# Kernel optimization log

Hardware: AMD Instinct MI355X
Metric: run time of the kernel (lower is better)

## Reference

```python
import jax, jax.numpy as jnp
import numpy as np

BETA = 0.25          # commitment loss weight (init kwarg)
CODEBOOK_SIZE = 2048


def setup_inputs() -> dict:
    key = jax.random.key(0)
    k1, k2 = jax.random.split(key)
    B, L, D = 8, 4096, 256
    z_e = jax.random.normal(k1, (B, L, D), dtype=jnp.float32)
    # xavier_uniform-style init for the codebook
    limit = float(np.sqrt(6.0 / (CODEBOOK_SIZE + D)))
    embed_weight = jax.random.uniform(k2, (CODEBOOK_SIZE, D), dtype=jnp.float32,
                                      minval=-limit, maxval=limit)
    return {"z_e": z_e, "embed_weight": embed_weight}


def reference(z_e, embed_weight):
    # eval-mode forward (no EMA buffer updates)
    B, L, D = z_e.shape
    K = embed_weight.shape[0]
    zf = z_e.reshape(-1, D)                                   # [N, D]
    d2 = (jnp.sum(zf * zf, axis=1, keepdims=True)
          - 2.0 * (zf @ embed_weight.T)
          + jnp.sum(embed_weight * embed_weight, axis=1)[None, :])
    distances = jnp.sqrt(jnp.maximum(d2, 0.0))                # [N, K]
    idx = jnp.argmin(distances, axis=1)                       # [N]
    z_q = embed_weight[idx].reshape(B, L, D)                  # gather

    commitment_loss = BETA * jnp.mean((jax.lax.stop_gradient(z_q) - z_e) ** 2)
    embedding_loss = jnp.mean((jax.lax.stop_gradient(z_e) - z_q) ** 2)

    # avg over one-hot encodings == normalized histogram of idx
    N = zf.shape[0]
    counts = jax.ops.segment_sum(jnp.ones((N,), jnp.float32), idx, num_segments=K)
    avg_probs = counts / N
    perplexity = jnp.exp(-jnp.sum(avg_probs * jnp.log(avg_probs + 1e-10)))
    vq_loss = commitment_loss + embedding_loss - 0.01 * perplexity

    z_q_st = z_e + jax.lax.stop_gradient(z_q - z_e)           # straight-through
    return z_q_st, vq_loss, idx.reshape(B, L)
```

## Files before the change

kernel.cpp:

```cpp
#include <hip/hip_runtime.h>
#include <math.h>

#define DDIM 256
#define NSPLIT 4
#define TILES_PER_SPLIT 16
#define TILE_CODES 32
#define TILE_BYTES 16384

typedef __attribute__((ext_vector_type(8))) short short8v;
typedef __attribute__((ext_vector_type(4))) float float4v;
typedef unsigned int u32;
typedef unsigned short u16;

__device__ __forceinline__ short f2bf(float x) {
    u32 u = __float_as_uint(x);
    u = u + 0x7fffu + ((u >> 16) & 1u);
    return (short)(u >> 16);
}

__device__ __forceinline__ void gload_lds16(const void* g, void* l) {
    __builtin_amdgcn_global_load_lds(
        (const __attribute__((address_space(1))) u32*)g,
        (__attribute__((address_space(3))) u32*)l, 16, 0, 0);
}

__device__ __forceinline__ float np_sq_chain(const float* v, int lane) {
    #pragma clang fp contract(off)
    const int half = lane >> 3, j = lane & 7;
    const float* base = v + half * 128 + j;
    float x = base[0];
    float c = x * x;
    #pragma unroll
    for (int m = 1; m < 16; ++m) {
        float y = base[8 * m];
        float s = y * y;
        c = c + s;
    }
    return c;
}

__device__ __forceinline__ float np_combine16(const float* c) {
    #pragma clang fp contract(off)
    float L = ((c[0] + c[1]) + (c[2] + c[3])) + ((c[4] + c[5]) + (c[6] + c[7]));
    float R = ((c[8] + c[9]) + (c[10] + c[11])) + ((c[12] + c[13]) + (c[14] + c[15]));
    return L + R;
}

__device__ __forceinline__ void ins3(float m, int k,
                                     float& v0, float& v1, float& v2,
                                     int& i0, int& i1, int& i2) {
    if (m < v0)      { v2 = v1; i2 = i1; v1 = v0; i1 = i0; v0 = m; i0 = k; }
    else if (m < v1) { v2 = v1; i2 = i1; v1 = m;  i1 = k; }
    else if (m < v2) { v2 = m;  i2 = k; }
}

__global__ void zero_counts_kernel(int* __restrict__ counts, int K) {
    int i = blockIdx.x * 256 + threadIdx.x;
    if (i < K) counts[i] = 0;
}

__global__ void code_norms_np_kernel(const float* __restrict__ e, float* __restrict__ e2) {
    __shared__ float buf[DDIM];
    __shared__ float ch[16];
    int k = blockIdx.x;
    int t = threadIdx.x;
    float4 v = *(const float4*)&e[(size_t)k * DDIM + t * 4];
    *(float4*)&buf[t * 4] = v;
    __syncthreads();
    if (t < 16) ch[t] = np_sq_chain(buf, t);
    __syncthreads();
    if (t == 0) e2[k] = np_combine16(ch);
}

__global__ void convert_permute_e_kernel(const float* __restrict__ e, char* __restrict__ ebf_p) {
    int id = blockIdx.x * 256 + threadIdx.x;
    int k = id >> 5, d8 = id & 31;
    const float* s = &e[(size_t)k * DDIM + d8 * 8];
    float4 f0 = *(const float4*)s;
    float4 f1 = *(const float4*)(s + 4);
    short8v v;
    v[0] = f2bf(f0.x); v[1] = f2bf(f0.y); v[2] = f2bf(f0.z); v[3] = f2bf(f0.w);
    v[4] = f2bf(f1.x); v[5] = f2bf(f1.y); v[6] = f2bf(f1.z); v[7] = f2bf(f1.w);
    *(short8v*)(ebf_p + ((size_t)(k >> 5) << 14) + d8 * 512 + (k & 31) * 16) = v;
}

__global__ __attribute__((amdgpu_flat_work_group_size(256, 256)))
__attribute__((amdgpu_waves_per_eu(4, 4)))
void vq_cand_kernel(const float* __restrict__ z, const char* __restrict__ ebf_p,
                    const float* __restrict__ e2, float* __restrict__ cand_v,
                    u16* __restrict__ cand_i) {
    __shared__ char smem[2][TILE_BYTES];
    const int t    = threadIdx.x;
    const int w    = t >> 6;
    const int lane = t & 63;
    const int quad = lane >> 4;
    const int l15  = lane & 15;
    const int s    = blockIdx.y;
    const int row0 = blockIdx.x * 64;
    const int rw0  = row0 + w * 16;

    const char* tile_base = ebf_p + (size_t)s * TILES_PER_SPLIT * TILE_BYTES;

    {
        const char* src = tile_base + w * 4096 + lane * 16;
        char* dst = smem[0] + w * 4096;
        #pragma unroll
        for (int q = 0; q < 4; ++q) gload_lds16(src + q * 1024, dst + q * 1024);
    }

    short8v zf[8];
    {
        const float* zr = &z[(size_t)(rw0 + l15) * DDIM];
        #pragma unroll
        for (int kk = 0; kk < 8; ++kk) {
            int d0 = kk * 32 + quad * 8;
            float4 f0 = *(const float4*)&zr[d0];
            float4 f1 = *(const float4*)&zr[d0 + 4];
            short8v v;
            v[0] = f2bf(f0.x); v[1] = f2bf(f0.y); v[2] = f2bf(f0.z); v[3] = f2bf(f0.w);
            v[4] = f2bf(f1.x); v[5] = f2bf(f1.y); v[6] = f2bf(f1.z); v[7] = f2bf(f1.w);
            zf[kk] = v;
        }
    }

    float v0 = 3.4e38f, v1 = 3.4e38f, v2 = 3.4e38f;
    int   i0 = 0x7fff,  i1 = 0x7fff,  i2 = 0x7fff;

    __syncthreads();

    #pragma unroll 1
    for (int tt = 0; tt < TILES_PER_SPLIT; ++tt) {
        if (tt + 1 < TILES_PER_SPLIT) {
            const char* src = tile_base + (size_t)(tt + 1) * TILE_BYTES + w * 4096 + lane * 16;
            char* dst = smem[(tt + 1) & 1] + w * 4096;
            #pragma unroll
            for (int q = 0; q < 4; ++q) gload_lds16(src + q * 1024, dst + q * 1024);
        }
        const char* es = smem[tt & 1];

        float4v acc0 = (float4v)0.0f, acc1 = (float4v)0.0f;

        #pragma unroll
        for (int kk = 0; kk < 8; ++kk) {
            int c = kk * 4 + quad;
            short8v a0 = *(const short8v*)(es + c * 512 + l15 * 16);
            short8v a1 = *(const short8v*)(es + c * 512 + (16 + l15) * 16);
            acc0 = __builtin_amdgcn_mfma_f32_16x16x32_bf16(a0, zf[kk], acc0, 0, 0, 0);
            acc1 = __builtin_amdgcn_mfma_f32_16x16x32_bf16(a1, zf[kk], acc1, 0, 0, 0);
        }

        const int kbase = s * 512 + tt * TILE_CODES;
        #pragma unroll
        for (int reg = 0; reg < 4; ++reg) {
            int cl0 = quad * 4 + reg;
            float m0 = fmaf(-2.0f, acc0[reg], e2[kbase + cl0]);
            ins3(m0, kbase + cl0, v0, v1, v2, i0, i1, i2);
            int cl1 = 16 + quad * 4 + reg;
            float m1 = fmaf(-2.0f, acc1[reg], e2[kbase + cl1]);
            ins3(m1, kbase + cl1, v0, v1, v2, i0, i1, i2);
        }
        __syncthreads();
    }

    {
        float bm0 = 3.4e38f, bm1 = 3.4e38f, bm2 = 3.4e38f;
        int   bk0 = 0x7fff,  bk1 = 0x7fff,  bk2 = 0x7fff;
        #pragma unroll
        for (int q = 0; q < 4; ++q) {
            int src = l15 + q * 16;
            float m0 = __shfl(v0, src); int k0 = __shfl(i0, src);
            float m1 = __shfl(v1, src); int k1 = __shfl(i1, src);
            float m2 = __shfl(v2, src); int k2 = __shfl(i2, src);
            ins3(m0, k0, bm0, bm1, bm2, bk0, bk1, bk2);
            ins3(m1, k1, bm0, bm1, bm2, bk0, bk1, bk2);
            ins3(m2, k2, bm0, bm1, bm2, bk0, bk1, bk2);
        }
        if (quad == 0) {
            size_t base = (size_t)(rw0 + l15) * 12 + s * 3;
            cand_v[base]     = bm0;  cand_i[base]     = (u16)bk0;
            cand_v[base + 1] = bm1;  cand_i[base + 1] = (u16)bk1;
            cand_v[base + 2] = bm2;  cand_i[base + 2] = (u16)bk2;
        }
    }
}

__global__ void refine_fused_kernel(const float* __restrict__ z, const float* __restrict__ e,
                                    const float* __restrict__ e2np,
                                    const float* __restrict__ cand_v,
                                    const u16* __restrict__ cand_i,
                                    int* __restrict__ counts, float* __restrict__ partials,
                                    float* __restrict__ out_zq, float* __restrict__ out_idx) {
    __shared__ float buf[4][DDIM];
    __shared__ float ch[4][16];
    __shared__ float wsum[4];
    const int w = threadIdx.x >> 6;
    const int t = threadIdx.x & 63;
    const int n = blockIdx.x * 4 + w;

    float4 zv = *(const float4*)&z[(size_t)n * DDIM + t * 4];
    *(float4*)&buf[w][t * 4] = zv;
    __syncthreads();
    if (t < 16) ch[w][t] = np_sq_chain(buf[w], t);
    __syncthreads();

    float bv[6]; int bi[6];
    #pragma unroll
    for (int c = 0; c < 6; ++c) { bv[c] = 3.4e38f; bi[c] = 0x7fffffff; }
    #pragma unroll
    for (int c = 0; c < 12; ++c) {
        float v  = cand_v[(size_t)n * 12 + c];
        int   id = (int)cand_i[(size_t)n * 12 + c];
        #pragma unroll
        for (int x = 0; x < 6; ++x) {
            if (v < bv[x] || (v == bv[x] && id < bi[x])) {
                for (int d = 5; d > x; --d) { bv[d] = bv[d - 1]; bi[d] = bi[d - 1]; }
                bv[x] = v; bi[x] = id;
                break;
            }
        }
    }

    float dotf[6];
    #pragma unroll
    for (int c = 0; c < 6; ++c) {
        int k = bi[c];
        float4 ev = *(const float4*)&e[(size_t)k * DDIM + t * 4];
        double p = (double)zv.x * (double)ev.x + (double)zv.y * (double)ev.y
                 + (double)zv.z * (double)ev.z + (double)zv.w * (double)ev.w;
        #pragma unroll
        for (int o = 32; o > 0; o >>= 1) p += __shfl_down(p, o);
        dotf[c] = (float)p;
    }

    int bk = 0;
    if (t == 0) {
        #pragma clang fp contract(off)
        float sx = np_combine16(ch[w]);
        float bd = 3.4e38f;
        bk = 0x7fffffff;
        #pragma unroll
        for (int c = 0; c < 6; ++c) {
            float twod = 2.0f * dotf[c];
            float t1 = sx - twod;
            float d2v = t1 + e2np[bi[c]];
            d2v = fmaxf(d2v, 0.0f);
            float d = sqrtf(d2v);
            if (d < bd || (d == bd && bi[c] < bk)) { bd = d; bk = bi[c]; }
        }
    }
    int wk = __shfl(bk, 0);

    float4 ev = *(const float4*)&e[(size_t)wk * DDIM + t * 4];
    *(float4*)&out_zq[(size_t)n * DDIM + t * 4] = ev;
    float dx = zv.x - ev.x, dy = zv.y - ev.y, dz = zv.z - ev.z, dw = zv.w - ev.w;
    float sq = dx * dx + dy * dy + dz * dz + dw * dw;
    #pragma unroll
    for (int o = 32; o > 0; o >>= 1) sq += __shfl_down(sq, o);
    if (t == 0) {
        wsum[w] = sq;
        atomicAdd(&counts[wk], 1);
        out_idx[n] = (float)wk;
    }
    __syncthreads();
    if (threadIdx.x == 0)
        partials[blockIdx.x] = wsum[0] + wsum[1] + wsum[2] + wsum[3];
}

__global__ void finalize_kernel(const int* __restrict__ counts, const float* __restrict__ partials,
                                float* __restrict__ out_loss, int K, int NB,
                                float invN, float invND) {
    int t = threadIdx.x;
    double ent = 0.0, sq = 0.0;
    for (int k = t; k < K; k += 256) {
        float p = (float)counts[k] * invN;
        ent += (double)(p * logf(p + 1e-10f));
    }
    for (int i = t; i < NB; i += 256) sq += (double)partials[i];
    #pragma unroll
    for (int o = 32; o > 0; o >>= 1) {
        ent += __shfl_down(ent, o);
        sq  += __shfl_down(sq, o);
    }
    __shared__ double e4[4], s4[4];
    if ((t & 63) == 0) { e4[t >> 6] = ent; s4[t >> 6] = sq; }
    __syncthreads();
    if (t == 0) {
        double esum = e4[0] + e4[1] + e4[2] + e4[3];
        double ssum = s4[0] + s4[1] + s4[2] + s4[3];
        float perp = expf((float)(-esum));
        float mean = (float)ssum * invND;
        out_loss[0] = 1.25f * mean - 0.01f * perp;
    }
}

extern "C" void kernel_launch(void* const* d_in, const int* in_sizes, int n_in,
                              void* d_out, int out_size, void* d_ws, size_t ws_size,
                              hipStream_t stream) {
    const float* z = (const float*)d_in[0];
    const float* e = (const float*)d_in[1];
    const int N = in_sizes[0] / DDIM;
    const int K = in_sizes[1] / DDIM;

    float* out      = (float*)d_out;
    float* out_zq   = out;
    float* out_loss = out + (size_t)N * DDIM;
    float* out_idx  = out_loss + 1;

    int*   counts   = (int*)d_ws;
    float* e2np     = (float*)((char*)d_ws + 8192);
    float* partials = (float*)((char*)d_ws + 16384);
    float* cand_v   = (float*)((char*)d_ws + 49152);
    u16*   cand_i   = (u16*)((char*)d_ws + 1622016);
    char*  ebf_p    = (char*)d_ws + 2408448;

    zero_counts_kernel<<<(K + 255) / 256, 256, 0, stream>>>(counts, K);
    code_norms_np_kernel<<<K, 64, 0, stream>>>(e, e2np);
    convert_permute_e_kernel<<<K * 32 / 256, 256, 0, stream>>>(e, ebf_p);
    vq_cand_kernel<<<dim3(N / 64, NSPLIT), 256, 0, stream>>>(z, ebf_p, e2np, cand_v, cand_i);
    refine_fused_kernel<<<N / 4, 256, 0, stream>>>(z, e, e2np, cand_v, cand_i,
                                                   counts, partials, out_zq, out_idx);
    finalize_kernel<<<1, 256, 0, stream>>>(counts, partials, out_loss, K, N / 4,
                                           1.0f / (float)N, 1.0f / (float)(N * DDIM));
}
```

Baseline: 455.6 us.

## Double rows per wave in candidate kernel with deeper async codebook prefetch

Each wave now handles 32 query rows instead of 16, so every codebook tile read from LDS feeds twice as many MFMAs, and the grid is halved. Codebook tiles are prefetched two ahead with explicit vmcnt waits and raw barriers instead of __syncthreads. Code norms are staged in LDS, and the candidate buffers switch to a split-major layout, with the refine kernel updated to read it. In exchange, register pressure rises from doubled accumulators and z fragments, and the hand-written waitcnt logic is easy to get wrong.

```diff
diff --git a/kernel.cpp b/kernel.cpp
--- a/kernel.cpp
+++ b/kernel.cpp
@@ -6,6 +6,7 @@
 #define TILES_PER_SPLIT 16
 #define TILE_CODES 32
 #define TILE_BYTES 16384
+#define ROWS_PER_BLOCK 128
 
 typedef __attribute__((ext_vector_type(8))) short short8v;
 typedef __attribute__((ext_vector_type(4))) float float4v;
@@ -88,95 +89,146 @@
 __attribute__((amdgpu_waves_per_eu(4, 4)))
 void vq_cand_kernel(const float* __restrict__ z, const char* __restrict__ ebf_p,
                     const float* __restrict__ e2, float* __restrict__ cand_v,
-                    u16* __restrict__ cand_i) {
-    __shared__ char smem[2][TILE_BYTES];
+                    u16* __restrict__ cand_i, int N) {
+    __shared__ __align__(16) char smem[2][TILE_BYTES];
+    __shared__ float e2s[512];
     const int t    = threadIdx.x;
     const int w    = t >> 6;
     const int lane = t & 63;
     const int quad = lane >> 4;
     const int l15  = lane & 15;
     const int s    = blockIdx.y;
-    const int row0 = blockIdx.x * 64;
-    const int rw0  = row0 + w * 16;
+    const int row0 = blockIdx.x * ROWS_PER_BLOCK;
+    const int rw0  = row0 + w * 32;
 
     const char* tile_base = ebf_p + (size_t)s * TILES_PER_SPLIT * TILE_BYTES;
 
     {
-        const char* src = tile_base + w * 4096 + lane * 16;
-        char* dst = smem[0] + w * 4096;
-        #pragma unroll
-        for (int q = 0; q < 4; ++q) gload_lds16(src + q * 1024, dst + q * 1024);
-    }
-
-    short8v zf[8];
+        const char* src0 = tile_base + w * 4096 + lane * 16;
+        char* dst0 = smem[0] + w * 4096;
+        char* dst1 = smem[1] + w * 4096;
+        #pragma unroll
+        for (int q = 0; q < 4; ++q) gload_lds16(src0 + q * 1024, dst0 + q * 1024);
+        #pragma unroll
+        for (int q = 0; q < 4; ++q) gload_lds16(src0 + TILE_BYTES + q * 1024, dst1 + q * 1024);
+    }
+
+    e2s[t]       = e2[s * 512 + t];
+    e2s[t + 256] = e2[s * 512 + t + 256];
+
+    short8v zf0[8], zf1[8];
     {
-        const float* zr = &z[(size_t)(rw0 + l15) * DDIM];
+        const float* zrA = &z[(size_t)(rw0 + l15) * DDIM];
         #pragma unroll
         for (int kk = 0; kk < 8; ++kk) {
             int d0 = kk * 32 + quad * 8;
-            float4 f0 = *(const float4*)&zr[d0];
-            float4 f1 = *(const float4*)&zr[d0 + 4];
+            float4 f0 = *(const float4*)&zrA[d0];
+            float4 f1 = *(const float4*)&zrA[d0 + 4];
             short8v v;
             v[0] = f2bf(f0.x); v[1] = f2bf(f0.y); v[2] = f2bf(f0.z); v[3] = f2bf(f0.w);
             v[4] = f2bf(f1.x); v[5] = f2bf(f1.y); v[6] = f2bf(f1.z); v[7] = f2bf(f1.w);
-            zf[kk] = v;
-        }
-    }
-
-    float v0 = 3.4e38f, v1 = 3.4e38f, v2 = 3.4e38f;
-    int   i0 = 0x7fff,  i1 = 0x7fff,  i2 = 0x7fff;
-
-    __syncthreads();
+            zf0[kk] = v;
+        }
+        const float* zrB = &z[(size_t)(rw0 + 16 + l15) * DDIM];
+        #pragma unroll
+        for (int kk = 0; kk < 8; ++kk) {
+            int d0 = kk * 32 + quad * 8;
+            float4 f0 = *(const float4*)&zrB[d0];
+            float4 f1 = *(const float4*)&zrB[d0 + 4];
+            short8v v;
+            v[0] = f2bf(f0.x); v[1] = f2bf(f0.y); v[2] = f2bf(f0.z); v[3] = f2bf(f0.w);
+            v[4] = f2bf(f1.x); v[5] = f2bf(f1.y); v[6] = f2bf(f1.z); v[7] = f2bf(f1.w);
+            zf1[kk] = v;
+        }
+    }
+
+    float va0 = 3.4e38f, va1 = 3.4e38f, va2 = 3.4e38f;
+    int   ia0 = 0x7fff,  ia1 = 0x7fff,  ia2 = 0x7fff;
+    float vb0 = 3.4e38f, vb1 = 3.4e38f, vb2 = 3.4e38f;
+    int   ib0 = 0x7fff,  ib1 = 0x7fff,  ib2 = 0x7fff;
+
+    asm volatile("s_waitcnt lgkmcnt(0)" ::: "memory");
 
     #pragma unroll 1
     for (int tt = 0; tt < TILES_PER_SPLIT; ++tt) {
-        if (tt + 1 < TILES_PER_SPLIT) {
-            const char* src = tile_base + (size_t)(tt + 1) * TILE_BYTES + w * 4096 + lane * 16;
-            char* dst = smem[(tt + 1) & 1] + w * 4096;
-            #pragma unroll
-            for (int q = 0; q < 4; ++q) gload_lds16(src + q * 1024, dst + q * 1024);
-        }
+        if (tt < TILES_PER_SPLIT - 1)
+            asm volatile("s_waitcnt vmcnt(4)" ::: "memory");
+        else
+            asm volatile("s_waitcnt vmcnt(0)" ::: "memory");
+        __builtin_amdgcn_s_barrier();
+
         const char* es = smem[tt & 1];
-
-        float4v acc0 = (float4v)0.0f, acc1 = (float4v)0.0f;
+        float4v acc00 = (float4v)0.0f, acc01 = (float4v)0.0f;
+        float4v acc10 = (float4v)0.0f, acc11 = (float4v)0.0f;
 
         #pragma unroll
         for (int kk = 0; kk < 8; ++kk) {
             int c = kk * 4 + quad;
             short8v a0 = *(const short8v*)(es + c * 512 + l15 * 16);
             short8v a1 = *(const short8v*)(es + c * 512 + (16 + l15) * 16);
-            acc0 = __builtin_amdgcn_mfma_f32_16x16x32_bf16(a0, zf[kk], acc0, 0, 0, 0);
-            acc1 = __builtin_amdgcn_mfma_f32_16x16x32_bf16(a1, zf[kk], acc1, 0, 0, 0);
-        }
-
-        const int kbase = s * 512 + tt * TILE_CODES;
+            acc00 = __builtin_amdgcn_mfma_f32_16x16x32_bf16(a0, zf0[kk], acc00, 0, 0, 0);
+            acc01 = __builtin_amdgcn_mfma_f32_16x16x32_bf16(a1, zf0[kk], acc01, 0, 0, 0);
+            acc10 = __builtin_amdgcn_mfma_f32_16x16x32_bf16(a0, zf1[kk], acc10, 0, 0, 0);
+            acc11 = __builtin_amdgcn_mfma_f32_16x16x32_bf16(a1, zf1[kk], acc11, 0, 0, 0);
+        }
+
+        const int kloc  = tt * TILE_CODES;
+        const int kbase = s * 512 + kloc;
         #pragma unroll
         for (int reg = 0; reg < 4; ++reg) {
             int cl0 = quad * 4 + reg;
-            float m0 = fmaf(-2.0f, acc0[reg], e2[kbase + cl0]);
-            ins3(m0, kbase + cl0, v0, v1, v2, i0, i1, i2);
             int cl1 = 16 + quad * 4 + reg;
-            float m1 = fmaf(-2.0f, acc1[reg], e2[kbase + cl1]);
-            ins3(m1, kbase + cl1, v0, v1, v2, i0, i1, i2);
-        }
-        __syncthreads();
+            float e20 = e2s[kloc + cl0];
+            float e21 = e2s[kloc + cl1];
+            float m00 = fmaf(-2.0f, acc00[reg], e20);
+            ins3(m00, kbase + cl0, va0, va1, va2, ia0, ia1, ia2);
+            float m01 = fmaf(-2.0f, acc01[reg], e21);
+            ins3(m01, kbase + cl1, va0, va1, va2, ia0, ia1, ia2);
+            float m10 = fmaf(-2.0f, acc10[reg], e20);
+            ins3(m10, kbase + cl0, vb0, vb1, vb2, ib0, ib1, ib2);
+            float m11 = fmaf(-2.0f, acc11[reg], e21);
+            ins3(m11, kbase + cl1, vb0, vb1, vb2, ib0, ib1, ib2);
+        }
+
+        asm volatile("s_waitcnt lgkmcnt(0)" ::: "memory");
+        __builtin_amdgcn_s_barrier();
+
+        if (tt + 2 < TILES_PER_SPLIT) {
+            const char* src = tile_base + (size_t)(tt + 2) * TILE_BYTES + w * 4096 + lane * 16;
+            char* dst = smem[tt & 1] + w * 4096;
+            #pragma unroll
+            for (int q = 0; q < 4; ++q) gload_lds16(src + q * 1024, dst + q * 1024);
+        }
     }
 
     {
+        float am0 = 3.4e38f, am1 = 3.4e38f, am2 = 3.4e38f;
+        int   ak0 = 0x7fff,  ak1 = 0x7fff,  ak2 = 0x7fff;
         float bm0 = 3.4e38f, bm1 = 3.4e38f, bm2 = 3.4e38f;
         int   bk0 = 0x7fff,  bk1 = 0x7fff,  bk2 = 0x7fff;
         #pragma unroll
         for (int q = 0; q < 4; ++q) {
             int src = l15 + q * 16;
-            float m0 = __shfl(v0, src); int k0 = __shfl(i0, src);
-            float m1 = __shfl(v1, src); int k1 = __shfl(i1, src);
-            float m2 = __shfl(v2, src); int k2 = __shfl(i2, src);
+            float m0 = __shfl(va0, src); int k0 = __shfl(ia0, src);
+            float m1 = __shfl(va1, src); int k1 = __shfl(ia1, src);
+            float m2 = __shfl(va2, src); int k2 = __shfl(ia2, src);
+            ins3(m0, k0, am0, am1, am2, ak0, ak1, ak2);
+            ins3(m1, k1, am0, am1, am2, ak0, ak1, ak2);
+            ins3(m2, k2, am0, am1, am2, ak0, ak1, ak2);
+            m0 = __shfl(vb0, src); k0 = __shfl(ib0, src);
+            m1 = __shfl(vb1, src); k1 = __shfl(ib1, src);
+            m2 = __shfl(vb2, src); k2 = __shfl(ib2, src);
             ins3(m0, k0, bm0, bm1, bm2, bk0, bk1, bk2);
             ins3(m1, k1, bm0, bm1, bm2, bk0, bk1, bk2);
             ins3(m2, k2, bm0, bm1, bm2, bk0, bk1, bk2);
         }
         if (quad == 0) {
-            size_t base = (size_t)(rw0 + l15) * 12 + s * 3;
+            size_t base = ((size_t)s * N + (rw0 + l15)) * 3;
+            cand_v[base]     = am0;  cand_i[base]     = (u16)ak0;
+            cand_v[base + 1] = am1;  cand_i[base + 1] = (u16)ak1;
+            cand_v[base + 2] = am2;  cand_i[base + 2] = (u16)ak2;
+        } else if (quad == 1) {
+            size_t base = ((size_t)s * N + (rw0 + 16 + l15)) * 3;
             cand_v[base]     = bm0;  cand_i[base]     = (u16)bk0;
             cand_v[base + 1] = bm1;  cand_i[base + 1] = (u16)bk1;
             cand_v[base + 2] = bm2;  cand_i[base + 2] = (u16)bk2;
@@ -189,7 +241,8 @@
                                     const float* __restrict__ cand_v,
                                     const u16* __restrict__ cand_i,
                                     int* __restrict__ counts, float* __restrict__ partials,
-                                    float* __restrict__ out_zq, float* __restrict__ out_idx) {
+                                    float* __restrict__ out_zq, float* __restrict__ out_idx,
+                                    int N) {
     __shared__ float buf[4][DDIM];
     __shared__ float ch[4][16];
     __shared__ float wsum[4];
@@ -208,8 +261,10 @@
     for (int c = 0; c < 6; ++c) { bv[c] = 3.4e38f; bi[c] = 0x7fffffff; }
     #pragma unroll
     for (int c = 0; c < 12; ++c) {
-        float v  = cand_v[(size_t)n * 12 + c];
-        int   id = (int)cand_i[(size_t)n * 12 + c];
+        int sp = c / 3, j = c - sp * 3;
+        size_t off = ((size_t)sp * N + n) * 3 + j;
+        float v  = cand_v[off];
+        int   id = (int)cand_i[off];
         #pragma unroll
         for (int x = 0; x < 6; ++x) {
             if (v < bv[x] || (v == bv[x] && id < bi[x])) {
@@ -316,9 +371,10 @@
     zero_counts_kernel<<<(K + 255) / 256, 256, 0, stream>>>(counts, K);
     code_norms_np_kernel<<<K, 64, 0, stream>>>(e, e2np);
     convert_permute_e_kernel<<<K * 32 / 256, 256, 0, stream>>>(e, ebf_p);
-    vq_cand_kernel<<<dim3(N / 64, NSPLIT), 256, 0, stream>>>(z, ebf_p, e2np, cand_v, cand_i);
+    vq_cand_kernel<<<dim3(N / ROWS_PER_BLOCK, NSPLIT), 256, 0, stream>>>(z, ebf_p, e2np,
+                                                                         cand_v, cand_i, N);
     refine_fused_kernel<<<N / 4, 256, 0, stream>>>(z, e, e2np, cand_v, cand_i,
-                                                   counts, partials, out_zq, out_idx);
+                                                   counts, partials, out_zq, out_idx, N);
     finalize_kernel<<<1, 256, 0, stream>>>(counts, partials, out_loss, K, N / 4,
                                            1.0f / (float)N, 1.0f / (float)(N * DDIM));
 }
```

After: 445.1 us. 2.3% less time.

## Keep whole codebook split resident in LDS and stream row groups through it

Applied to the files above, without the earlier changes.

The candidate search now uses 1024-thread blocks that load an entire 256-code bf16 split (128KB) plus its norms into LDS once, then loop over four groups of 256 rows without per-tile double buffering or barriers. The split count doubles to 8, so refine now merges 24 candidates per row from a split-major layout. The goal is to cut repeated codebook traffic and barrier overhead per row. In exchange, the large LDS footprint limits each CU to one block, the grid becomes 32x8 blocks, and refine does more candidate merging.

```diff
diff --git a/kernel.cpp b/kernel.cpp
--- a/kernel.cpp
+++ b/kernel.cpp
@@ -2,10 +2,12 @@
 #include <math.h>
 
 #define DDIM 256
-#define NSPLIT 4
-#define TILES_PER_SPLIT 16
+#define NSPLIT 8
+#define TILES_PER_SPLIT 8
 #define TILE_CODES 32
 #define TILE_BYTES 16384
+#define SPLIT_BYTES (TILES_PER_SPLIT * TILE_BYTES)
+#define ROWS_PER_BLOCK 1024
 
 typedef __attribute__((ext_vector_type(8))) short short8v;
 typedef __attribute__((ext_vector_type(4))) float float4v;
@@ -84,85 +86,81 @@
     *(short8v*)(ebf_p + ((size_t)(k >> 5) << 14) + d8 * 512 + (k & 31) * 16) = v;
 }
 
-__global__ __attribute__((amdgpu_flat_work_group_size(256, 256)))
+__global__ __attribute__((amdgpu_flat_work_group_size(1024, 1024)))
 __attribute__((amdgpu_waves_per_eu(4, 4)))
 void vq_cand_kernel(const float* __restrict__ z, const char* __restrict__ ebf_p,
                     const float* __restrict__ e2, float* __restrict__ cand_v,
-                    u16* __restrict__ cand_i) {
-    __shared__ char smem[2][TILE_BYTES];
+                    u16* __restrict__ cand_i, int N) {
+    __shared__ __align__(16) char codes[SPLIT_BYTES];
+    __shared__ float e2s[256];
     const int t    = threadIdx.x;
     const int w    = t >> 6;
     const int lane = t & 63;
     const int quad = lane >> 4;
     const int l15  = lane & 15;
     const int s    = blockIdx.y;
-    const int row0 = blockIdx.x * 64;
-    const int rw0  = row0 + w * 16;
-
-    const char* tile_base = ebf_p + (size_t)s * TILES_PER_SPLIT * TILE_BYTES;
+    const int row0 = blockIdx.x * ROWS_PER_BLOCK;
 
     {
-        const char* src = tile_base + w * 4096 + lane * 16;
-        char* dst = smem[0] + w * 4096;
-        #pragma unroll
-        for (int q = 0; q < 4; ++q) gload_lds16(src + q * 1024, dst + q * 1024);
-    }
-
-    short8v zf[8];
-    {
-        const float* zr = &z[(size_t)(rw0 + l15) * DDIM];
-        #pragma unroll
-        for (int kk = 0; kk < 8; ++kk) {
-            int d0 = kk * 32 + quad * 8;
-            float4 f0 = *(const float4*)&zr[d0];
-            float4 f1 = *(const float4*)&zr[d0 + 4];
-            short8v v;
-            v[0] = f2bf(f0.x); v[1] = f2bf(f0.y); v[2] = f2bf(f0.z); v[3] = f2bf(f0.w);
-            v[4] = f2bf(f1.x); v[5] = f2bf(f1.y); v[6] = f2bf(f1.z); v[7] = f2bf(f1.w);
-            zf[kk] = v;
-        }
-    }
-
-    float v0 = 3.4e38f, v1 = 3.4e38f, v2 = 3.4e38f;
-    int   i0 = 0x7fff,  i1 = 0x7fff,  i2 = 0x7fff;
-
+        const char* src = ebf_p + (size_t)s * SPLIT_BYTES + w * 1024 + lane * 16;
+        char* dst = codes + w * 1024;
+        #pragma unroll
+        for (int r = 0; r < 8; ++r) gload_lds16(src + r * 16384, dst + r * 16384);
+    }
+    if (t < 256) e2s[t] = e2[s * 256 + t];
     __syncthreads();
 
     #pragma unroll 1
-    for (int tt = 0; tt < TILES_PER_SPLIT; ++tt) {
-        if (tt + 1 < TILES_PER_SPLIT) {
-            const char* src = tile_base + (size_t)(tt + 1) * TILE_BYTES + w * 4096 + lane * 16;
-            char* dst = smem[(tt + 1) & 1] + w * 4096;
+    for (int g = 0; g < 4; ++g) {
+        const int rw = row0 + g * 256 + w * 16;
+
+        short8v zf[8];
+        {
+            const float* zr = &z[(size_t)(rw + l15) * DDIM];
             #pragma unroll
-            for (int q = 0; q < 4; ++q) gload_lds16(src + q * 1024, dst + q * 1024);
-        }
-        const char* es = smem[tt & 1];
-
-        float4v acc0 = (float4v)0.0f, acc1 = (float4v)0.0f;
-
-        #pragma unroll
-        for (int kk = 0; kk < 8; ++kk) {
-            int c = kk * 4 + quad;
-            short8v a0 = *(const short8v*)(es + c * 512 + l15 * 16);
-            short8v a1 = *(const short8v*)(es + c * 512 + (16 + l15) * 16);
-            acc0 = __builtin_amdgcn_mfma_f32_16x16x32_bf16(a0, zf[kk], acc0, 0, 0, 0);
-            acc1 = __builtin_amdgcn_mfma_f32_16x16x32_bf16(a1, zf[kk], acc1, 0, 0, 0);
-        }
-
-        const int kbase = s * 512 + tt * TILE_CODES;
-        #pragma unroll
-        for (int reg = 0; reg < 4; ++reg) {
-            int cl0 = quad * 4 + reg;
-            float m0 = fmaf(-2.0f, acc0[reg], e2[kbase + cl0]);
-            ins3(m0, kbase + cl0, v0, v1, v2, i0, i1, i2);
-            int cl1 = 16 + quad * 4 + reg;
-            float m1 = fmaf(-2.0f, acc1[reg], e2[kbase + cl1]);
-            ins3(m1, kbase + cl1, v0, v1, v2, i0, i1, i2);
-        }
-        __syncthreads();
-    }
-
-    {
+            for (int kk = 0; kk < 8; ++kk) {
+                int d0 = kk * 32 + quad * 8;
+                float4 f0 = *(const float4*)&zr[d0];
+                float4 f1 = *(const float4*)&zr[d0 + 4];
+                short8v v;
+                v[0] = f2bf(f0.x); v[1] = f2bf(f0.y); v[2] = f2bf(f0.z); v[3] = f2bf(f0.w);
+                v[4] = f2bf(f1.x); v[5] = f2bf(f1.y); v[6] = f2bf(f1.z); v[7] = f2bf(f1.w);
+                zf[kk] = v;
+            }
+        }
+
+        float v0 = 3.4e38f, v1 = 3.4e38f, v2 = 3.4e38f;
+        int   i0 = 0x7fff,  i1 = 0x7fff,  i2 = 0x7fff;
+
+        #pragma unroll
+        for (int tt = 0; tt < TILES_PER_SPLIT; ++tt) {
+            const char* es = codes + tt * TILE_BYTES;
+            float4v acc0 = (float4v)0.0f, acc1 = (float4v)0.0f;
+
+            #pragma unroll
+            for (int kk = 0; kk < 8; ++kk) {
+                int c = kk * 4 + quad;
+                short8v a0 = *(const short8v*)(es + c * 512 + l15 * 16);
+                short8v a1 = *(const short8v*)(es + c * 512 + (16 + l15) * 16);
+                acc0 = __builtin_amdgcn_mfma_f32_16x16x32_bf16(a0, zf[kk], acc0, 0, 0, 0);
+                acc1 = __builtin_amdgcn_mfma_f32_16x16x32_bf16(a1, zf[kk], acc1, 0, 0, 0);
+            }
+
+            const int kloc  = tt * TILE_CODES;
+            const int kbase = s * 256 + kloc;
+            float4 e2a = *(const float4*)&e2s[kloc + quad * 4];
+            float4 e2b = *(const float4*)&e2s[kloc + 16 + quad * 4];
+            float m;
+            m = fmaf(-2.0f, acc0[0], e2a.x); ins3(m, kbase + quad * 4 + 0,      v0, v1, v2, i0, i1, i2);
+            m = fmaf(-2.0f, acc1[0], e2b.x); ins3(m, kbase + 16 + quad * 4 + 0, v0, v1, v2, i0, i1, i2);
+            m = fmaf(-2.0f, acc0[1], e2a.y); ins3(m, kbase + quad * 4 + 1,      v0, v1, v2, i0, i1, i2);
+            m = fmaf(-2.0f, acc1[1], e2b.y); ins3(m, kbase + 16 + quad * 4 + 1, v0, v1, v2, i0, i1, i2);
+            m = fmaf(-2.0f, acc0[2], e2a.z); ins3(m, kbase + quad * 4 + 2,      v0, v1, v2, i0, i1, i2);
+            m = fmaf(-2.0f, acc1[2], e2b.z); ins3(m, kbase + 16 + quad * 4 + 2, v0, v1, v2, i0, i1, i2);
+            m = fmaf(-2.0f, acc0[3], e2a.w); ins3(m, kbase + quad * 4 + 3,      v0, v1, v2, i0, i1, i2);
+            m = fmaf(-2.0f, acc1[3], e2b.w); ins3(m, kbase + 16 + quad * 4 + 3, v0, v1, v2, i0, i1, i2);
+        }
+
         float bm0 = 3.4e38f, bm1 = 3.4e38f, bm2 = 3.4e38f;
         int   bk0 = 0x7fff,  bk1 = 0x7fff,  bk2 = 0x7fff;
         #pragma unroll
@@ -176,7 +174,7 @@
             ins3(m2, k2, bm0, bm1, bm2, bk0, bk1, bk2);
         }
         if (quad == 0) {
-            size_t base = (size_t)(rw0 + l15) * 12 + s * 3;
+            size_t base = ((size_t)s * N + (rw + l15)) * 3;
             cand_v[base]     = bm0;  cand_i[base]     = (u16)bk0;
             cand_v[base + 1] = bm1;  cand_i[base + 1] = (u16)bk1;
             cand_v[base + 2] = bm2;  cand_i[base + 2] = (u16)bk2;
@@ -189,7 +187,8 @@
                                     const float* __restrict__ cand_v,
                                     const u16* __restrict__ cand_i,
                                     int* __restrict__ counts, float* __restrict__ partials,
-                                    float* __restrict__ out_zq, float* __restrict__ out_idx) {
+                                    float* __restrict__ out_zq, float* __restrict__ out_idx,
+                                    int N) {
     __shared__ float buf[4][DDIM];
     __shared__ float ch[4][16];
     __shared__ float wsum[4];
@@ -207,9 +206,11 @@
     #pragma unroll
     for (int c = 0; c < 6; ++c) { bv[c] = 3.4e38f; bi[c] = 0x7fffffff; }
     #pragma unroll
-    for (int c = 0; c < 12; ++c) {
-        float v  = cand_v[(size_t)n * 12 + c];
-        int   id = (int)cand_i[(size_t)n * 12 + c];
+    for (int c = 0; c < 24; ++c) {
+        int sp = c / 3, j = c - sp * 3;
+        size_t off = ((size_t)sp * N + n) * 3 + j;
+        float v  = cand_v[off];
+        int   id = (int)cand_i[off];
         #pragma unroll
         for (int x = 0; x < 6; ++x) {
             if (v < bv[x] || (v == bv[x] && id < bi[x])) {
@@ -310,15 +311,16 @@
     float* e2np     = (float*)((char*)d_ws + 8192);
     float* partials = (float*)((char*)d_ws + 16384);
     float* cand_v   = (float*)((char*)d_ws + 49152);
-    u16*   cand_i   = (u16*)((char*)d_ws + 1622016);
-    char*  ebf_p    = (char*)d_ws + 2408448;
+    u16*   cand_i   = (u16*)((char*)d_ws + 3194880);
+    char*  ebf_p    = (char*)d_ws + 4767744;
 
     zero_counts_kernel<<<(K + 255) / 256, 256, 0, stream>>>(counts, K);
     code_norms_np_kernel<<<K, 64, 0, stream>>>(e, e2np);
     convert_permute_e_kernel<<<K * 32 / 256, 256, 0, stream>>>(e, ebf_p);
-    vq_cand_kernel<<<dim3(N / 64, NSPLIT), 256, 0, stream>>>(z, ebf_p, e2np, cand_v, cand_i);
+    vq_cand_kernel<<<dim3(N / ROWS_PER_BLOCK, NSPLIT), 1024, 0, stream>>>(z, ebf_p, e2np,
+                                                                          cand_v, cand_i, N);
     refine_fused_kernel<<<N / 4, 256, 0, stream>>>(z, e, e2np, cand_v, cand_i,
-                                                   counts, partials, out_zq, out_idx);
+                                                   counts, partials, out_zq, out_idx, N);
     finalize_kernel<<<1, 256, 0, stream>>>(counts, partials, out_loss, K, N / 4,
                                            1.0f / (float)N, 1.0f / (float)(N * DDIM));
 }
```

New measurement: 569.4 us. 1.25x slower.
